# Performance work log

Hardware: AMD Instinct MI355X
Metric: run time of the kernel (lower is better)

## Reference

```python
import jax, jax.numpy as jnp
import numpy as np
import math

L, D, NH, DFF, RPE = 6, 256, 8, 1024, 512
HD = D // NH
B, NQ = 2, 300
FH, FW = 64, 64
N = FH * FW
STRIDE = 16
SCALE = 1.0 / math.sqrt(HD)


def _ln(x, w, b, eps=1e-5):
    m = jnp.mean(x, -1, keepdims=True)
    v = jnp.mean((x - m) ** 2, -1, keepdims=True)
    return (x - m) * jax.lax.rsqrt(v + eps) * w + b


def _mha_self(x, pos, in_w, in_b, out_w, out_b):
    # torch nn.MultiheadAttention with packed in_proj, q=k=x+pos, v=x
    qk = x + pos
    wq, wk, wv = jnp.split(in_w, 3, 0)
    bq, bk, bv = jnp.split(in_b, 3, 0)
    q = (qk @ wq.T + bq).reshape(B, NQ, NH, HD)
    k = (qk @ wk.T + bk).reshape(B, NQ, NH, HD)
    v = (x @ wv.T + bv).reshape(B, NQ, NH, HD)
    a = jax.nn.softmax(jnp.einsum('bqhd,bkhd->bhqk', q, k) * SCALE, -1)
    o = jnp.einsum('bhqk,bkhd->bqhd', a, v).reshape(B, NQ, D)
    return o @ out_w.T + out_b


def _cross(q_in, box, k_in, v_in, qw, qb, kw, kb, vw, vb, pw, pb,
           c1w1, c1b1, c1w2, c2w1, c2b1, c2w2):
    # box: [B,NQ,1,4] xyxy in absolute pixels; learned relative position bias
    pos_x = (jnp.arange(FW, dtype=jnp.float32) + 0.5) * STRIDE  # linspace(0.5,w-0.5,w)*stride
    pos_y = (jnp.arange(FH, dtype=jnp.float32) + 0.5) * STRIDE
    dx = box[..., 0::2] - pos_x[None, None, :, None]  # [B,NQ,FW,2]
    dy = box[..., 1::2] - pos_y[None, None, :, None]  # [B,NQ,FH,2]
    rpe_x = jax.nn.relu(dx @ c1w1.T + c1b1) @ c1w2.T  # [B,NQ,FW,NH]
    rpe_y = jax.nn.relu(dy @ c2w1.T + c2b1) @ c2w2.T  # [B,NQ,FH,NH]
    rpe = (rpe_y[:, :, :, None, :] + rpe_x[:, :, None, :, :]).reshape(B, NQ, N, NH)
    q = ((q_in @ qw.T + qb) * SCALE).reshape(B, NQ, NH, HD)
    k = (k_in @ kw.T + kb).reshape(B, N, NH, HD)
    v = (v_in @ vw.T + vb).reshape(B, N, NH, HD)
    attn = jnp.einsum('bqhd,bkhd->bhqk', q, k) + rpe.transpose(0, 3, 1, 2)
    a = jax.nn.softmax(attn, -1)
    o = jnp.einsum('bhqk,bkhd->bqhd', a, v).reshape(B, NQ, D)
    return o @ pw.T + pb


def _decoder(tgt, query_pos, reference_points, src, src_pos_embed,
             sa_in_w, sa_in_b, sa_out_w, sa_out_b, n1_w, n1_b,
             ca_q_w, ca_q_b, ca_k_w, ca_k_b, ca_v_w, ca_v_b, ca_proj_w, ca_proj_b,
             cpb1_w1, cpb1_b1, cpb1_w2, cpb2_w1, cpb2_b1, cpb2_w2,
             n2_w, n2_b, ffn_w1, ffn_b1, ffn_w2, ffn_b2, n3_w, n3_b):
    ref = reference_points[:, :, None]  # [B,NQ,1,4] cxcywh
    box = jnp.concatenate([ref[..., :2] - ref[..., 2:] * 0.5,
                           ref[..., :2] + ref[..., 2:] * 0.5], -1)
    kv = src + src_pos_embed
    out = tgt
    for i in range(L):  # post-norm decoder layers, dropout=0 (eval)
        t = _mha_self(out, query_pos, sa_in_w[i], sa_in_b[i], sa_out_w[i], sa_out_b[i])
        out = _ln(out + t, n1_w[i], n1_b[i])
        t = _cross(out + query_pos, box, kv, src,
                   ca_q_w[i], ca_q_b[i], ca_k_w[i], ca_k_b[i], ca_v_w[i], ca_v_b[i],
                   ca_proj_w[i], ca_proj_b[i], cpb1_w1[i], cpb1_b1[i], cpb1_w2[i],
                   cpb2_w1[i], cpb2_b1[i], cpb2_w2[i])
        out = _ln(out + t, n2_w[i], n2_b[i])
        t = jax.nn.relu(out @ ffn_w1[i].T + ffn_b1[i]) @ ffn_w2[i].T + ffn_b2[i]
        out = _ln(out + t, n3_w[i], n3_b[i])
    return out


def setup_inputs() -> dict:
    key = jax.random.key(0)
    ks = iter(jax.random.split(key, 64))
    def w(*shape, s=0.02):
        return jax.random.normal(next(ks), shape, jnp.float32) * s
    inp = {}
    inp['tgt'] = w(B, NQ, D, s=1.0)
    inp['query_pos'] = w(B, NQ, D, s=1.0)
    cxcy = jax.random.uniform(next(ks), (B, NQ, 2)) * (FW * STRIDE)
    wh = jax.random.uniform(next(ks), (B, NQ, 2)) * 256.0 + 16.0
    inp['reference_points'] = jnp.concatenate([cxcy, wh], -1)
    inp['src'] = w(B, N, D, s=1.0)
    inp['src_pos_embed'] = w(B, N, D, s=1.0)
    inp['src_spatial_shapes'] = jnp.array([[FH, FW]], jnp.int32)
    inp['sa_in_w'] = w(L, 3 * D, D); inp['sa_in_b'] = jnp.zeros((L, 3 * D))
    inp['sa_out_w'] = w(L, D, D); inp['sa_out_b'] = jnp.zeros((L, D))
    inp['n1_w'] = jnp.ones((L, D)); inp['n1_b'] = jnp.zeros((L, D))
    inp['ca_q_w'] = w(L, D, D); inp['ca_q_b'] = jnp.zeros((L, D))
    inp['ca_k_w'] = w(L, D, D); inp['ca_k_b'] = jnp.zeros((L, D))
    inp['ca_v_w'] = w(L, D, D); inp['ca_v_b'] = jnp.zeros((L, D))
    inp['ca_proj_w'] = w(L, D, D); inp['ca_proj_b'] = jnp.zeros((L, D))
    inp['cpb1_w1'] = w(L, RPE, 2, s=0.001); inp['cpb1_b1'] = jnp.zeros((L, RPE))
    inp['cpb1_w2'] = w(L, NH, RPE, s=0.001)
    inp['cpb2_w1'] = w(L, RPE, 2, s=0.001); inp['cpb2_b1'] = jnp.zeros((L, RPE))
    inp['cpb2_w2'] = w(L, NH, RPE, s=0.001)
    inp['n2_w'] = jnp.ones((L, D)); inp['n2_b'] = jnp.zeros((L, D))
    inp['ffn_w1'] = w(L, DFF, D); inp['ffn_b1'] = jnp.zeros((L, DFF))
    inp['ffn_w2'] = w(L, D, DFF); inp['ffn_b2'] = jnp.zeros((L, D))
    inp['n3_w'] = jnp.ones((L, D)); inp['n3_b'] = jnp.zeros((L, D))
    return inp


def reference(tgt, query_pos, reference_points, src, src_pos_embed, src_spatial_shapes,
              sa_in_w, sa_in_b, sa_out_w, sa_out_b, n1_w, n1_b,
              ca_q_w, ca_q_b, ca_k_w, ca_k_b, ca_v_w, ca_v_b, ca_proj_w, ca_proj_b,
              cpb1_w1, cpb1_b1, cpb1_w2, cpb2_w1, cpb2_b1, cpb2_w2,
              n2_w, n2_b, ffn_w1, ffn_b1, ffn_w2, ffn_b2, n3_w, n3_b):
    # src_spatial_shapes is static ([[FH, FW]]); dims closed over as constants.
    return _decoder(tgt, query_pos, reference_points, src, src_pos_embed,
                    sa_in_w, sa_in_b, sa_out_w, sa_out_b, n1_w, n1_b,
                    ca_q_w, ca_q_b, ca_k_w, ca_k_b, ca_v_w, ca_v_b, ca_proj_w, ca_proj_b,
                    cpb1_w1, cpb1_b1, cpb1_w2, cpb2_w1, cpb2_b1, cpb2_w2,
                    n2_w, n2_b, ffn_w1, ffn_b1, ffn_w2, ffn_b2, n3_w, n3_b)
```

## Files before the change

kernel.cpp:

```cpp
#include <hip/hip_runtime.h>
#include <math.h>

#define NQ   300
#define DMODEL 256
#define NHEAD 8
#define HDIM 32
#define BB   2
#define NKV  4096
#define RPEH 512
#define NLAYER 6
#define ATTN_SCALE 0.17677669529663687f

typedef short short8 __attribute__((ext_vector_type(8)));
typedef float f32x4 __attribute__((ext_vector_type(4)));
typedef unsigned short ushort_t;

__device__ __forceinline__ short f2bf(float f) {
    union { float fv; unsigned u; } v; v.fv = f;
    unsigned r = v.u + 0x7FFFu + ((v.u >> 16) & 1u);
    return (short)(r >> 16);
}
__device__ __forceinline__ float bf2f(ushort_t u) {
    union { unsigned u; float f; } v; v.u = ((unsigned)u) << 16;
    return v.f;
}
__device__ __forceinline__ short8 pack_bf8(float4 x, float4 y) {
    short8 v;
    v[0] = f2bf(x.x); v[1] = f2bf(x.y); v[2] = f2bf(x.z); v[3] = f2bf(x.w);
    v[4] = f2bf(y.x); v[5] = f2bf(y.y); v[6] = f2bf(y.z); v[7] = f2bf(y.w);
    return v;
}

__global__ __launch_bounds__(256) void prep_kernel(
    const float* __restrict__ src, const float* __restrict__ spe,
    const float* __restrict__ tgt, const float* __restrict__ qpos,
    const float* __restrict__ refp,
    ushort_t* __restrict__ kvb16, ushort_t* __restrict__ srcb16,
    float* __restrict__ outb, ushort_t* __restrict__ ob16,
    ushort_t* __restrict__ oq16,
    float* __restrict__ boxx, float* __restrict__ boxy)
{
    int i = blockIdx.x * 256 + threadIdx.x;
    if (i < BB * NKV * DMODEL) {
        float s = src[i];
        kvb16[i]  = (ushort_t)f2bf(s + spe[i]);
        srcb16[i] = (ushort_t)f2bf(s);
    }
    if (i < BB * NQ * DMODEL) {
        float tv = tgt[i];
        outb[i] = tv;
        ob16[i] = (ushort_t)f2bf(tv);
        oq16[i] = (ushort_t)f2bf(tv + qpos[i]);
    }
    if (i < BB * NQ) {
        float cx = refp[i * 4 + 0], cy = refp[i * 4 + 1];
        float w  = refp[i * 4 + 2], h  = refp[i * 4 + 3];
        boxx[i * 2 + 0] = cx - 0.5f * w;
        boxx[i * 2 + 1] = cx + 0.5f * w;
        boxy[i * 2 + 0] = cy - 0.5f * h;
        boxy[i * 2 + 1] = cy + 0.5f * h;
    }
}

__global__ __launch_bounds__(256) void wconv_kernel(
    const float* __restrict__ sain, const float* __restrict__ saout,
    const float* __restrict__ caq, const float* __restrict__ cak,
    const float* __restrict__ cav, const float* __restrict__ cap,
    const float* __restrict__ f1, const float* __restrict__ f2,
    ushort_t* __restrict__ dst)
{
    size_t i = ((size_t)blockIdx.x * 256 + threadIdx.x) * 8;
    if (i >= 6291456) return;
    const float* s; size_t off;
    if      (i < 1179648) { s = sain;  off = i; }
    else if (i < 1572864) { s = saout; off = i - 1179648; }
    else if (i < 1966080) { s = caq;   off = i - 1572864; }
    else if (i < 2359296) { s = cak;   off = i - 1966080; }
    else if (i < 2752512) { s = cav;   off = i - 2359296; }
    else if (i < 3145728) { s = cap;   off = i - 2752512; }
    else if (i < 4718592) { s = f1;    off = i - 3145728; }
    else                  { s = f2;    off = i - 4718592; }
    float4 x = *(const float4*)&s[off];
    float4 y = *(const float4*)&s[off + 4];
    *(short8*)&dst[i] = pack_bf8(x, y);
}

__global__ __launch_bounds__(256) void kv_mega(
    const ushort_t* __restrict__ kvb16, const ushort_t* __restrict__ srcb16,
    const ushort_t* __restrict__ Wk, const ushort_t* __restrict__ Wv,
    const float* __restrict__ kbias, const float* __restrict__ vbias,
    ushort_t* __restrict__ Kcb, ushort_t* __restrict__ Vcb)
{
    __shared__ short A_s[64][264];
    const int t = threadIdx.x;
    const int lane = t & 63, w = t >> 6;
    const int wr = w >> 1, wc = w & 1;
    const int l15 = lane & 15, lhi8 = (lane >> 4) * 8;
    const int n0 = blockIdx.x * 64;
    const int m0 = blockIdx.y * 64;
    const int sel = blockIdx.z;
    const ushort_t* A  = sel ? srcb16 : kvb16;
    const ushort_t* Wb = sel ? Wv : Wk;
    const float* bb    = sel ? vbias : kbias;
    ushort_t* Cb       = sel ? Vcb : Kcb;

    {
        int row = t >> 2, c0 = (t & 3) * 64;
        const ushort_t* ap = &A[(size_t)(m0 + row) * 256 + c0];
#pragma unroll
        for (int c8 = 0; c8 < 8; ++c8)
            *(short8*)&A_s[row][c0 + c8 * 8] = *(const short8*)(ap + c8 * 8);
    }
    __syncthreads();

    const int ar0 = wr * 32 + l15, ar1 = ar0 + 16;
    const int rowb = m0 + wr * 32 + (lane >> 4) * 4;
    const int colb = n0 + wc * 32 + l15;

    for (int l = 0; l < NLAYER; ++l) {
        const ushort_t* wp0 = &Wb[(size_t)l * 65536 + (size_t)(n0 + wc * 32 + l15) * 256 + lhi8];
        const ushort_t* wp1 = wp0 + 16 * 256;
        f32x4 acc[2][2];
#pragma unroll
        for (int i = 0; i < 2; ++i)
#pragma unroll
            for (int j = 0; j < 2; ++j)
#pragma unroll
                for (int r = 0; r < 4; ++r) acc[i][j][r] = 0.f;
#pragma unroll
        for (int k0 = 0; k0 < 256; k0 += 32) {
            short8 a0 = *(short8*)&A_s[ar0][k0 + lhi8];
            short8 a1 = *(short8*)&A_s[ar1][k0 + lhi8];
            short8 b0 = *(const short8*)(wp0 + k0);
            short8 b1 = *(const short8*)(wp1 + k0);
            acc[0][0] = __builtin_amdgcn_mfma_f32_16x16x32_bf16(a0, b0, acc[0][0], 0, 0, 0);
            acc[0][1] = __builtin_amdgcn_mfma_f32_16x16x32_bf16(a0, b1, acc[0][1], 0, 0, 0);
            acc[1][0] = __builtin_amdgcn_mfma_f32_16x16x32_bf16(a1, b0, acc[1][0], 0, 0, 0);
            acc[1][1] = __builtin_amdgcn_mfma_f32_16x16x32_bf16(a1, b1, acc[1][1], 0, 0, 0);
        }
        ushort_t* C = Cb + (size_t)l * (BB * NKV * DMODEL);
        const float* bl = bb + l * 256;
#pragma unroll
        for (int ni = 0; ni < 2; ++ni) {
            int col = colb + ni * 16;
            float bv = bl[col];
#pragma unroll
            for (int mi = 0; mi < 2; ++mi)
#pragma unroll
                for (int r = 0; r < 4; ++r) {
                    int row = rowb + mi * 16 + r;
                    C[(size_t)row * 256 + col] = (ushort_t)f2bf(acc[mi][ni][r] + bv);
                }
        }
    }
}

template<int OUT_BF16, int RELU>
__global__ __launch_bounds__(256) void gemm_direct(
    const ushort_t* __restrict__ A1, const ushort_t* __restrict__ A2, int plimit,
    int lda, const ushort_t* __restrict__ W, const float* __restrict__ bias,
    void* __restrict__ Cv, int ldc, int M, int K, float scale, int slimit)
{
    const int t = threadIdx.x;
    const int lane = t & 63, w = t >> 6;
    const int wr = w >> 1, wc = w & 1;
    const int l15 = lane & 15, lhi8 = (lane >> 4) * 8;
    const int m0 = blockIdx.y * 64, n0 = blockIdx.x * 64;
    const ushort_t* A = (n0 < plimit) ? A1 : A2;

    int r0 = m0 + wr * 32 + l15;      if (r0 > M - 1) r0 = M - 1;
    int r1 = m0 + wr * 32 + 16 + l15; if (r1 > M - 1) r1 = M - 1;
    const ushort_t* ap0 = &A[(size_t)r0 * lda + lhi8];
    const ushort_t* ap1 = &A[(size_t)r1 * lda + lhi8];
    const ushort_t* wp0 = &W[(size_t)(n0 + wc * 32 + l15) * K + lhi8];
    const ushort_t* wp1 = wp0 + (size_t)16 * K;

    f32x4 acc[2][2];
#pragma unroll
    for (int i = 0; i < 2; ++i)
#pragma unroll
        for (int j = 0; j < 2; ++j)
#pragma unroll
            for (int r = 0; r < 4; ++r) acc[i][j][r] = 0.f;

    for (int k0 = 0; k0 < K; k0 += 32) {
        short8 a0 = *(const short8*)(ap0 + k0);
        short8 a1 = *(const short8*)(ap1 + k0);
        short8 b0 = *(const short8*)(wp0 + k0);
        short8 b1 = *(const short8*)(wp1 + k0);
        acc[0][0] = __builtin_amdgcn_mfma_f32_16x16x32_bf16(a0, b0, acc[0][0], 0, 0, 0);
        acc[0][1] = __builtin_amdgcn_mfma_f32_16x16x32_bf16(a0, b1, acc[0][1], 0, 0, 0);
        acc[1][0] = __builtin_amdgcn_mfma_f32_16x16x32_bf16(a1, b0, acc[1][0], 0, 0, 0);
        acc[1][1] = __builtin_amdgcn_mfma_f32_16x16x32_bf16(a1, b1, acc[1][1], 0, 0, 0);
    }

    const int rowb = m0 + wr * 32 + (lane >> 4) * 4;
    const int colb = n0 + wc * 32 + l15;
#pragma unroll
    for (int ni = 0; ni < 2; ++ni) {
        int col = colb + ni * 16;
        float bv = bias[col];
#pragma unroll
        for (int mi = 0; mi < 2; ++mi)
#pragma unroll
            for (int r = 0; r < 4; ++r) {
                int row = rowb + mi * 16 + r;
                if (row < M) {
                    float v = acc[mi][ni][r] + bv;
                    if (col < slimit) v *= scale;
                    if (RELU) v = fmaxf(v, 0.f);
                    if (OUT_BF16)
                        ((ushort_t*)Cv)[(size_t)row * ldc + col] = (ushort_t)f2bf(v);
                    else
                        ((float*)Cv)[(size_t)row * ldc + col] = v;
                }
            }
    }
}

__global__ __launch_bounds__(256) void ln_residual(
    float* __restrict__ out, const float* __restrict__ tt,
    const float* __restrict__ qpos,
    const float* __restrict__ w, const float* __restrict__ b,
    ushort_t* __restrict__ ob16, ushort_t* __restrict__ oq16, int rows)
{
    const int wid = threadIdx.x >> 6, lane = threadIdx.x & 63;
    const int row = blockIdx.x * 4 + wid;
    if (row >= rows) return;
    const float* orow = out + row * DMODEL;
    const float* trow = tt + row * DMODEL;
    float x[4];
#pragma unroll
    for (int i = 0; i < 4; ++i) x[i] = orow[lane + 64 * i] + trow[lane + 64 * i];
    float s = x[0] + x[1] + x[2] + x[3];
#pragma unroll
    for (int mask = 1; mask < 64; mask <<= 1) s += __shfl_xor(s, mask);
    float mean = s * (1.f / 256.f);
    float vs = 0.f;
#pragma unroll
    for (int i = 0; i < 4; ++i) { float d = x[i] - mean; vs += d * d; }
#pragma unroll
    for (int mask = 1; mask < 64; mask <<= 1) vs += __shfl_xor(vs, mask);
    float r = rsqrtf(vs * (1.f / 256.f) + 1e-5f);
    float* orw = out + row * DMODEL;
#pragma unroll
    for (int i = 0; i < 4; ++i) {
        int c = lane + 64 * i;
        float val = (x[i] - mean) * r * w[c] + b[c];
        orw[c] = val;
        ob16[row * DMODEL + c] = (ushort_t)f2bf(val);
        oq16[row * DMODEL + c] = (ushort_t)f2bf(val + qpos[row * DMODEL + c]);
    }
}

__global__ __launch_bounds__(256) void rpe_all(
    const float* __restrict__ boxx, const float* __restrict__ boxy,
    const float* __restrict__ cpb1_w1, const float* __restrict__ cpb1_b1,
    const float* __restrict__ cpb1_w2,
    const float* __restrict__ cpb2_w1, const float* __restrict__ cpb2_b1,
    const float* __restrict__ cpb2_w2,
    float* __restrict__ rx6, float* __restrict__ ry6)
{
    __shared__ float wb_s[RPEH][4];
    __shared__ float w2_s[RPEH][8];

    const int axis = blockIdx.y;
    const int l = blockIdx.z;
    const float* __restrict__ w1 = (axis ? cpb2_w1 : cpb1_w1) + (size_t)l * 1024;
    const float* __restrict__ b1 = (axis ? cpb2_b1 : cpb1_b1) + (size_t)l * 512;
    const float* __restrict__ w2 = (axis ? cpb2_w2 : cpb1_w2) + (size_t)l * 4096;
    const float* __restrict__ bx = axis ? boxy : boxx;
    const int t = threadIdx.x;

    for (int j = t; j < RPEH; j += 256) {
        wb_s[j][0] = w1[2 * j];
        wb_s[j][1] = w1[2 * j + 1];
        wb_s[j][2] = b1[j];
        wb_s[j][3] = 0.f;
#pragma unroll
        for (int h = 0; h < 8; ++h) w2_s[j][h] = w2[h * RPEH + j];
    }
    __syncthreads();

    const int row = blockIdx.x * 256 + t;
    const int i  = row & 63;
    const int bq = row >> 6;
    const float pos = (i + 0.5f) * 16.0f;
    const float d0 = bx[bq * 2 + 0] - pos;
    const float d1 = bx[bq * 2 + 1] - pos;

    float acc[8];
#pragma unroll
    for (int h = 0; h < 8; ++h) acc[h] = 0.f;

#pragma unroll 4
    for (int j = 0; j < RPEH; ++j) {
        float4 wb = *(const float4*)&wb_s[j][0];
        float hv = fmaxf(fmaf(d0, wb.x, fmaf(d1, wb.y, wb.z)), 0.f);
        float4 a = *(const float4*)&w2_s[j][0];
        float4 c = *(const float4*)&w2_s[j][4];
        acc[0] = fmaf(hv, a.x, acc[0]);
        acc[1] = fmaf(hv, a.y, acc[1]);
        acc[2] = fmaf(hv, a.z, acc[2]);
        acc[3] = fmaf(hv, a.w, acc[3]);
        acc[4] = fmaf(hv, c.x, acc[4]);
        acc[5] = fmaf(hv, c.y, acc[5]);
        acc[6] = fmaf(hv, c.z, acc[6]);
        acc[7] = fmaf(hv, c.w, acc[7]);
    }

    const int b = bq / NQ, q = bq % NQ;
    float* __restrict__ dst = (axis ? ry6 : rx6) + (size_t)l * 307200;
#pragma unroll
    for (int h = 0; h < 8; ++h)
        dst[((size_t)(b * NHEAD + h) * NQ + q) * 64 + i] = acc[h];
}

template<int HAS_RPE>
__global__ __launch_bounds__(256) void attn_mfma(
    const ushort_t* __restrict__ Q, int ldq,
    const ushort_t* __restrict__ K, int ldk,
    const ushort_t* __restrict__ V, int ldv,
    int nkeys, int kps,
    const float* __restrict__ RX, const float* __restrict__ RY,
    ushort_t* __restrict__ po, float* __restrict__ pm, float* __restrict__ pl,
    int nsplit)
{
    __shared__ short Q_s[64][40];
    __shared__ short K_s[64][40];
    __shared__ short V_s[32][72];
    __shared__ short P_s[4][16][72];

    const int t = threadIdx.x;
    const int lane = t & 63, w = t >> 6;
    const int l15 = lane & 15, lhi8 = (lane >> 4) * 8, lhi4 = (lane >> 4) * 4;
    const int bh = blockIdx.y, b = bh >> 3, h = bh & 7;
    const int q0 = blockIdx.x * 64;
    const int sp = blockIdx.z;

    {
        int q = t >> 2, kc = (t & 3) * 8;
        int qi = q0 + q;
        short8 qv = {0,0,0,0,0,0,0,0};
        if (qi < NQ) qv = *(const short8*)&Q[((size_t)(b * NQ + qi)) * ldq + h * HDIM + kc];
        *(short8*)&Q_s[q][kc] = qv;
    }

    float rxv[4][4];
    const float* ryp[4];
    if (HAS_RPE) {
#pragma unroll
        for (int r = 0; r < 4; ++r) {
            int qi = q0 + w * 16 + lhi4 + r;
            int qc = qi < NQ ? qi : NQ - 1;
            const float* rxp = &RX[((size_t)bh * NQ + qc) * 64];
            ryp[r] = &RY[((size_t)bh * NQ + qc) * 64];
#pragma unroll
            for (int nf = 0; nf < 4; ++nf) rxv[r][nf] = rxp[nf * 16 + l15];
        }
    }

    float m_r[4], l_r[4];
    f32x4 oacc[2];
#pragma unroll
    for (int r = 0; r < 4; ++r) { m_r[r] = -1e30f; l_r[r] = 0.f; }
#pragma unroll
    for (int ni = 0; ni < 2; ++ni)
#pragma unroll
        for (int r = 0; r < 4; ++r) oacc[ni][r] = 0.f;

    const int nt = kps >> 6;
    for (int kt = 0; kt < nt; ++kt) {
        const int key0 = sp * kps + (kt << 6);
        __syncthreads();
        {
            int key = t >> 2, kc = (t & 3) * 8;
            int rk = key0 + key;
            int rkc = rk < nkeys ? rk : nkeys - 1;
            short8 kvv = *(const short8*)&K[((size_t)(b * nkeys + rkc)) * ldk + h * HDIM + kc];
            *(short8*)&K_s[key][kc] = kvv;
            short8 vvv = *(const short8*)&V[((size_t)(b * nkeys + rkc)) * ldv + h * HDIM + kc];
#pragma unroll
            for (int j = 0; j < 8; ++j) V_s[kc + j][key] = vvv[j];
        }
        __syncthreads();

        short8 aq = *(short8*)&Q_s[w * 16 + l15][lhi8];
        f32x4 sacc[4];
#pragma unroll
        for (int nf = 0; nf < 4; ++nf) {
#pragma unroll
            for (int r = 0; r < 4; ++r) sacc[nf][r] = 0.f;
            short8 kb = *(short8*)&K_s[nf * 16 + l15][lhi8];
            sacc[nf] = __builtin_amdgcn_mfma_f32_16x16x32_bf16(aq, kb, sacc[nf], 0, 0, 0);
        }

        const int ktg = key0 >> 6;
        const bool kv0 = key0 +      l15 < nkeys;
        const bool kv1 = key0 + 16 + l15 < nkeys;
        const bool kv2 = key0 + 32 + l15 < nkeys;
        const bool kv3 = key0 + 48 + l15 < nkeys;
        float c_r[4];
#pragma unroll
        for (int r = 0; r < 4; ++r) {
            float ryv = HAS_RPE ? ryp[r][ktg] : 0.f;
            float sv0 = sacc[0][r] + ryv, sv1 = sacc[1][r] + ryv;
            float sv2 = sacc[2][r] + ryv, sv3 = sacc[3][r] + ryv;
            if (HAS_RPE) {
                sv0 += rxv[r][0]; sv1 += rxv[r][1];
                sv2 += rxv[r][2]; sv3 += rxv[r][3];
            }
            sv0 = kv0 ? sv0 : -1e30f;
            sv1 = kv1 ? sv1 : -1e30f;
            sv2 = kv2 ? sv2 : -1e30f;
            sv3 = kv3 ? sv3 : -1e30f;
            float tmax = fmaxf(fmaxf(sv0, sv1), fmaxf(sv2, sv3));
#pragma unroll
            for (int mask = 1; mask < 16; mask <<= 1)
                tmax = fmaxf(tmax, __shfl_xor(tmax, mask));
            float mn = fmaxf(m_r[r], tmax);
            float cc = __expf(m_r[r] - mn);
            m_r[r] = mn; c_r[r] = cc;
            float p0 = __expf(sv0 - mn), p1 = __expf(sv1 - mn);
            float p2 = __expf(sv2 - mn), p3 = __expf(sv3 - mn);
            float ps = p0 + p1 + p2 + p3;
#pragma unroll
            for (int mask = 1; mask < 16; mask <<= 1) ps += __shfl_xor(ps, mask);
            l_r[r] = l_r[r] * cc + ps;
            P_s[w][lhi4 + r][     l15] = f2bf(p0);
            P_s[w][lhi4 + r][16 + l15] = f2bf(p1);
            P_s[w][lhi4 + r][32 + l15] = f2bf(p2);
            P_s[w][lhi4 + r][48 + l15] = f2bf(p3);
        }
#pragma unroll
        for (int ni = 0; ni < 2; ++ni)
#pragma unroll
            for (int r = 0; r < 4; ++r) oacc[ni][r] *= c_r[r];

        short8 pa0 = *(short8*)&P_s[w][l15][lhi8];
        short8 pa1 = *(short8*)&P_s[w][l15][32 + lhi8];
#pragma unroll
        for (int ni = 0; ni < 2; ++ni) {
            short8 vb0 = *(short8*)&V_s[ni * 16 + l15][lhi8];
            short8 vb1 = *(short8*)&V_s[ni * 16 + l15][32 + lhi8];
            oacc[ni] = __builtin_amdgcn_mfma_f32_16x16x32_bf16(pa0, vb0, oacc[ni], 0, 0, 0);
            oacc[ni] = __builtin_amdgcn_mfma_f32_16x16x32_bf16(pa1, vb1, oacc[ni], 0, 0, 0);
        }
    }

#pragma unroll
    for (int r = 0; r < 4; ++r) {
        int qi = q0 + w * 16 + lhi4 + r;
        if (qi < NQ) {
            size_t base = ((size_t)(bh * nsplit + sp) * NQ + qi);
            if (l15 == 0) { pm[base] = m_r[r]; pl[base] = l_r[r]; }
            po[base * 32 + l15] = (ushort_t)f2bf(oacc[0][r]);
            po[base * 32 + 16 + l15] = (ushort_t)f2bf(oacc[1][r]);
        }
    }
}

__global__ __launch_bounds__(256) void combine_gemm(
    const ushort_t* __restrict__ po, const float* __restrict__ pm,
    const float* __restrict__ pl, int nsplit,
    const ushort_t* __restrict__ W, const float* __restrict__ bias,
    float* __restrict__ C, int M)
{
    __shared__ short A_s2[64][264];
    const int t = threadIdx.x;
    const int m0 = blockIdx.y * 64, n0 = blockIdx.x * 64;

    {
        int rloc = t >> 2;
        int row = m0 + rloc;
        int dc = (t & 3) * 64;
        if (row < M) {
            int b = row / NQ, q = row % NQ;
#pragma unroll
            for (int hh = 0; hh < 2; ++hh) {
                int h = (dc >> 5) + hh;
                int bh = b * NHEAD + h;
                float Mx = -1e30f;
                for (int s = 0; s < nsplit; ++s)
                    Mx = fmaxf(Mx, pm[(size_t)(bh * nsplit + s) * NQ + q]);
                float L = 0.f;
                float acc[32];
#pragma unroll
                for (int d = 0; d < 32; ++d) acc[d] = 0.f;
                for (int s = 0; s < nsplit; ++s) {
                    size_t base = (size_t)(bh * nsplit + s) * NQ + q;
                    float wgt = __expf(pm[base] - Mx);
                    L += pl[base] * wgt;
                    const ushort_t* pp = &po[base * 32];
#pragma unroll
                    for (int d = 0; d < 32; ++d) acc[d] += bf2f(pp[d]) * wgt;
                }
                float inv = 1.f / L;
#pragma unroll
                for (int d = 0; d < 32; ++d)
                    A_s2[rloc][dc + hh * 32 + d] = f2bf(acc[d] * inv);
            }
        } else {
#pragma unroll
            for (int d = 0; d < 64; ++d) A_s2[rloc][dc + d] = 0;
        }
    }
    __syncthreads();

    const int lane = t & 63, w = t >> 6;
    const int wr = w >> 1, wc = w & 1;
    const int l15 = lane & 15, lhi8 = (lane >> 4) * 8;
    const ushort_t* wp0 = &W[(size_t)(n0 + wc * 32 + l15) * 256 + lhi8];
    const ushort_t* wp1 = wp0 + 16 * 256;
    f32x4 acc[2][2];
#pragma unroll
    for (int i = 0; i < 2; ++i)
#pragma unroll
        for (int j = 0; j < 2; ++j)
#pragma unroll
            for (int r = 0; r < 4; ++r) acc[i][j][r] = 0.f;

#pragma unroll
    for (int k0 = 0; k0 < 256; k0 += 32) {
        short8 a0 = *(short8*)&A_s2[wr * 32 + l15][k0 + lhi8];
        short8 a1 = *(short8*)&A_s2[wr * 32 + 16 + l15][k0 + lhi8];
        short8 b0 = *(const short8*)(wp0 + k0);
        short8 b1 = *(const short8*)(wp1 + k0);
        acc[0][0] = __builtin_amdgcn_mfma_f32_16x16x32_bf16(a0, b0, acc[0][0], 0, 0, 0);
        acc[0][1] = __builtin_amdgcn_mfma_f32_16x16x32_bf16(a0, b1, acc[0][1], 0, 0, 0);
        acc[1][0] = __builtin_amdgcn_mfma_f32_16x16x32_bf16(a1, b0, acc[1][0], 0, 0, 0);
        acc[1][1] = __builtin_amdgcn_mfma_f32_16x16x32_bf16(a1, b1, acc[1][1], 0, 0, 0);
    }

    const int rowb = m0 + wr * 32 + (lane >> 4) * 4;
    const int colb = n0 + wc * 32 + l15;
#pragma unroll
    for (int ni = 0; ni < 2; ++ni) {
        int col = colb + ni * 16;
        float bv = bias[col];
#pragma unroll
        for (int mi = 0; mi < 2; ++mi)
#pragma unroll
            for (int r = 0; r < 4; ++r) {
                int row = rowb + mi * 16 + r;
                if (row < M)
                    C[(size_t)row * 256 + col] = acc[mi][ni][r] + bv;
            }
    }
}

extern "C" void kernel_launch(void* const* d_in, const int* in_sizes, int n_in,
                              void* d_out, int out_size, void* d_ws, size_t ws_size,
                              hipStream_t stream)
{
    const float* tgt   = (const float*)d_in[0];
    const float* qpos  = (const float*)d_in[1];
    const float* refp  = (const float*)d_in[2];
    const float* src   = (const float*)d_in[3];
    const float* spe   = (const float*)d_in[4];
    const float* sa_in_w  = (const float*)d_in[6];
    const float* sa_in_b  = (const float*)d_in[7];
    const float* sa_out_w = (const float*)d_in[8];
    const float* sa_out_b = (const float*)d_in[9];
    const float* n1_w  = (const float*)d_in[10];
    const float* n1_b  = (const float*)d_in[11];
    const float* ca_q_w = (const float*)d_in[12];
    const float* ca_q_b = (const float*)d_in[13];
    const float* ca_k_w = (const float*)d_in[14];
    const float* ca_k_b = (const float*)d_in[15];
    const float* ca_v_w = (const float*)d_in[16];
    const float* ca_v_b = (const float*)d_in[17];
    const float* ca_p_w = (const float*)d_in[18];
    const float* ca_p_b = (const float*)d_in[19];
    const float* cpb1_w1 = (const float*)d_in[20];
    const float* cpb1_b1 = (const float*)d_in[21];
    const float* cpb1_w2 = (const float*)d_in[22];
    const float* cpb2_w1 = (const float*)d_in[23];
    const float* cpb2_b1 = (const float*)d_in[24];
    const float* cpb2_w2 = (const float*)d_in[25];
    const float* n2_w = (const float*)d_in[26];
    const float* n2_b = (const float*)d_in[27];
    const float* ffn_w1 = (const float*)d_in[28];
    const float* ffn_b1 = (const float*)d_in[29];
    const float* ffn_w2 = (const float*)d_in[30];
    const float* ffn_b2 = (const float*)d_in[31];
    const float* n3_w = (const float*)d_in[32];
    const float* n3_b = (const float*)d_in[33];

    float* ws  = (float*)d_ws;
    float* outb = ws;
    float* tb   = outb + 153600;
    float* rx6  = tb + 153600;
    float* ry6  = rx6 + 1843200;
    float* boxx = ry6 + 1843200;
    float* boxy = boxx + 1200;
    float* pm   = boxy + 1200;
    float* pl   = pm + 38400;
    ushort_t* u = (ushort_t*)(pl + 38400);
    ushort_t* qkvb   = u;
    ushort_t* qcb    = qkvb + 460800;
    ushort_t* ob16   = qcb + 153600;
    ushort_t* oq16   = ob16 + 153600;
    ushort_t* hbb    = oq16 + 153600;
    ushort_t* poh    = hbb + 614400;
    ushort_t* kvb16  = poh + 1228800;
    ushort_t* srcb16 = kvb16 + 2097152;
    ushort_t* Kcb    = srcb16 + 2097152;
    ushort_t* Vcb    = Kcb + 12582912;
    ushort_t* Wseg   = Vcb + 12582912;
    ushort_t* Wsain  = Wseg;
    ushort_t* Wsaout = Wsain + 1179648;
    ushort_t* Wcaq   = Wsaout + 393216;
    ushort_t* Wcak   = Wcaq + 393216;
    ushort_t* Wcav   = Wcak + 393216;
    ushort_t* Wcap   = Wcav + 393216;
    ushort_t* Wff1   = Wcap + 393216;
    ushort_t* Wff2   = Wff1 + 1572864;

    const int M = BB * NQ;

    prep_kernel<<<8192, 256, 0, stream>>>(src, spe, tgt, qpos, refp,
        kvb16, srcb16, outb, ob16, oq16, boxx, boxy);
    wconv_kernel<<<3072, 256, 0, stream>>>(sa_in_w, sa_out_w, ca_q_w, ca_k_w,
        ca_v_w, ca_p_w, ffn_w1, ffn_w2, Wseg);
    rpe_all<<<dim3(150, 2, 6), 256, 0, stream>>>(boxx, boxy,
        cpb1_w1, cpb1_b1, cpb1_w2, cpb2_w1, cpb2_b1, cpb2_w2, rx6, ry6);
    kv_mega<<<dim3(4, 128, 2), 256, 0, stream>>>(kvb16, srcb16, Wcak, Wcav,
        ca_k_b, ca_v_b, Kcb, Vcb);

    for (int l = 0; l < NLAYER; ++l) {
        gemm_direct<1,0><<<dim3(12, 10), 256, 0, stream>>>(
            oq16, ob16, 512, 256, Wsain + (size_t)l * 196608, sa_in_b + (size_t)l * 768,
            qkvb, 768, M, 256, ATTN_SCALE, 256);
        attn_mfma<0><<<dim3(5, 16, 5), 256, 0, stream>>>(
            qkvb, 768, qkvb + 256, 768, qkvb + 512, 768,
            NQ, 64, nullptr, nullptr, poh, pm, pl, 5);
        combine_gemm<<<dim3(4, 10), 256, 0, stream>>>(
            poh, pm, pl, 5, Wsaout + (size_t)l * 65536, sa_out_b + l * 256, tb, M);
        ln_residual<<<150, 256, 0, stream>>>(outb, tb, qpos,
            n1_w + l * 256, n1_b + l * 256, ob16, oq16, M);

        gemm_direct<1,0><<<dim3(4, 10), 256, 0, stream>>>(
            oq16, oq16, 256, 256, Wcaq + (size_t)l * 65536, ca_q_b + l * 256,
            qcb, 256, M, 256, ATTN_SCALE, 256);
        attn_mfma<1><<<dim3(5, 16, 8), 256, 0, stream>>>(
            qcb, 256, Kcb + (size_t)l * 2097152, 256, Vcb + (size_t)l * 2097152, 256,
            NKV, 512, rx6 + (size_t)l * 307200, ry6 + (size_t)l * 307200,
            poh, pm, pl, 8);
        combine_gemm<<<dim3(4, 10), 256, 0, stream>>>(
            poh, pm, pl, 8, Wcap + (size_t)l * 65536, ca_p_b + l * 256, tb, M);
        ln_residual<<<150, 256, 0, stream>>>(outb, tb, qpos,
            n2_w + l * 256, n2_b + l * 256, ob16, oq16, M);

        gemm_direct<1,1><<<dim3(16, 10), 256, 0, stream>>>(
            ob16, ob16, 1024, 256, Wff1 + (size_t)l * 262144, ffn_b1 + l * 1024,
            hbb, 1024, M, 256, 1.f, 0);
        gemm_direct<0,0><<<dim3(4, 10), 256, 0, stream>>>(
            hbb, hbb, 256, 1024, Wff2 + (size_t)l * 262144, ffn_b2 + l * 256,
            tb, 256, M, 1024, 1.f, 0);
        ln_residual<<<150, 256, 0, stream>>>(outb, tb, qpos,
            n3_w + l * 256, n3_b + l * 256, ob16, oq16, M);
    }

    hipMemcpyAsync(d_out, outb, (size_t)M * DMODEL * sizeof(float),
                   hipMemcpyDeviceToDevice, stream);
}
```

Baseline: 866.4 us.

## Fuse output projections with residual LayerNorm and restructure RPE MLP evaluation

The attention output projections and the second FFN GEMM now each compute a full 64x256 row tile per block and apply residual add plus LayerNorm in the same kernel. This removes the separate ln_residual launches and the round trip of the intermediate tensor through global memory, 18 launches in total. In exchange the grid shrinks from 40 blocks to 10 for these GEMMs, so far fewer compute units are used. The RPE kernel now has each thread evaluate 8 consecutive positions by stepping the pre-activation linearly, which cuts the first-layer math and enables vectorised stores, but launches far fewer blocks.

```diff
diff --git a/kernel.cpp b/kernel.cpp
--- a/kernel.cpp
+++ b/kernel.cpp
@@ -218,41 +218,6 @@
     }
 }
 
-__global__ __launch_bounds__(256) void ln_residual(
-    float* __restrict__ out, const float* __restrict__ tt,
-    const float* __restrict__ qpos,
-    const float* __restrict__ w, const float* __restrict__ b,
-    ushort_t* __restrict__ ob16, ushort_t* __restrict__ oq16, int rows)
-{
-    const int wid = threadIdx.x >> 6, lane = threadIdx.x & 63;
-    const int row = blockIdx.x * 4 + wid;
-    if (row >= rows) return;
-    const float* orow = out + row * DMODEL;
-    const float* trow = tt + row * DMODEL;
-    float x[4];
-#pragma unroll
-    for (int i = 0; i < 4; ++i) x[i] = orow[lane + 64 * i] + trow[lane + 64 * i];
-    float s = x[0] + x[1] + x[2] + x[3];
-#pragma unroll
-    for (int mask = 1; mask < 64; mask <<= 1) s += __shfl_xor(s, mask);
-    float mean = s * (1.f / 256.f);
-    float vs = 0.f;
-#pragma unroll
-    for (int i = 0; i < 4; ++i) { float d = x[i] - mean; vs += d * d; }
-#pragma unroll
-    for (int mask = 1; mask < 64; mask <<= 1) vs += __shfl_xor(vs, mask);
-    float r = rsqrtf(vs * (1.f / 256.f) + 1e-5f);
-    float* orw = out + row * DMODEL;
-#pragma unroll
-    for (int i = 0; i < 4; ++i) {
-        int c = lane + 64 * i;
-        float val = (x[i] - mean) * r * w[c] + b[c];
-        orw[c] = val;
-        ob16[row * DMODEL + c] = (ushort_t)f2bf(val);
-        oq16[row * DMODEL + c] = (ushort_t)f2bf(val + qpos[row * DMODEL + c]);
-    }
-}
-
 __global__ __launch_bounds__(256) void rpe_all(
     const float* __restrict__ boxx, const float* __restrict__ boxy,
     const float* __restrict__ cpb1_w1, const float* __restrict__ cpb1_b1,
@@ -282,38 +247,53 @@
     }
     __syncthreads();
 
-    const int row = blockIdx.x * 256 + t;
-    const int i  = row & 63;
-    const int bq = row >> 6;
-    const float pos = (i + 0.5f) * 16.0f;
-    const float d0 = bx[bq * 2 + 0] - pos;
-    const float d1 = bx[bq * 2 + 1] - pos;
-
-    float acc[8];
-#pragma unroll
-    for (int h = 0; h < 8; ++h) acc[h] = 0.f;
-
-#pragma unroll 4
+    const int bq = blockIdx.x * 32 + (t >> 3);
+    const int i0 = (t & 7) * 8;
+    const bool valid = bq < BB * NQ;
+    const int bqc = valid ? bq : BB * NQ - 1;
+    const float pos0 = (i0 + 0.5f) * 16.0f;
+    const float d0 = bx[bqc * 2 + 0] - pos0;
+    const float d1 = bx[bqc * 2 + 1] - pos0;
+
+    float acc[8][8];
+#pragma unroll
+    for (int e = 0; e < 8; ++e)
+#pragma unroll
+        for (int h = 0; h < 8; ++h) acc[e][h] = 0.f;
+
+#pragma unroll 2
     for (int j = 0; j < RPEH; ++j) {
         float4 wb = *(const float4*)&wb_s[j][0];
-        float hv = fmaxf(fmaf(d0, wb.x, fmaf(d1, wb.y, wb.z)), 0.f);
-        float4 a = *(const float4*)&w2_s[j][0];
-        float4 c = *(const float4*)&w2_s[j][4];
-        acc[0] = fmaf(hv, a.x, acc[0]);
-        acc[1] = fmaf(hv, a.y, acc[1]);
-        acc[2] = fmaf(hv, a.z, acc[2]);
-        acc[3] = fmaf(hv, a.w, acc[3]);
-        acc[4] = fmaf(hv, c.x, acc[4]);
-        acc[5] = fmaf(hv, c.y, acc[5]);
-        acc[6] = fmaf(hv, c.z, acc[6]);
-        acc[7] = fmaf(hv, c.w, acc[7]);
-    }
-
-    const int b = bq / NQ, q = bq % NQ;
-    float* __restrict__ dst = (axis ? ry6 : rx6) + (size_t)l * 307200;
-#pragma unroll
-    for (int h = 0; h < 8; ++h)
-        dst[((size_t)(b * NHEAD + h) * NQ + q) * 64 + i] = acc[h];
+        float a = fmaf(d0, wb.x, fmaf(d1, wb.y, wb.z));
+        float s = 16.0f * (wb.x + wb.y);
+        float4 w2a = *(const float4*)&w2_s[j][0];
+        float4 w2b = *(const float4*)&w2_s[j][4];
+        float tv = a;
+#pragma unroll
+        for (int e = 0; e < 8; ++e) {
+            float hv = fmaxf(tv, 0.f);
+            acc[e][0] = fmaf(hv, w2a.x, acc[e][0]);
+            acc[e][1] = fmaf(hv, w2a.y, acc[e][1]);
+            acc[e][2] = fmaf(hv, w2a.z, acc[e][2]);
+            acc[e][3] = fmaf(hv, w2a.w, acc[e][3]);
+            acc[e][4] = fmaf(hv, w2b.x, acc[e][4]);
+            acc[e][5] = fmaf(hv, w2b.y, acc[e][5]);
+            acc[e][6] = fmaf(hv, w2b.z, acc[e][6]);
+            acc[e][7] = fmaf(hv, w2b.w, acc[e][7]);
+            tv -= s;
+        }
+    }
+
+    if (valid) {
+        const int b = bq / NQ, q = bq % NQ;
+        float* __restrict__ dst = (axis ? ry6 : rx6) + (size_t)l * 307200;
+#pragma unroll
+        for (int h = 0; h < 8; ++h) {
+            float* p = &dst[((size_t)(b * NHEAD + h) * NQ + q) * 64 + i0];
+            *(float4*)p       = make_float4(acc[0][h], acc[1][h], acc[2][h], acc[3][h]);
+            *(float4*)(p + 4) = make_float4(acc[4][h], acc[5][h], acc[6][h], acc[7][h]);
+        }
+    }
 }
 
 template<int HAS_RPE>
@@ -460,15 +440,18 @@
     }
 }
 
-__global__ __launch_bounds__(256) void combine_gemm(
+__global__ __launch_bounds__(256) void combine_gemm_ln(
     const ushort_t* __restrict__ po, const float* __restrict__ pm,
     const float* __restrict__ pl, int nsplit,
     const ushort_t* __restrict__ W, const float* __restrict__ bias,
-    float* __restrict__ C, int M)
+    float* __restrict__ outb, const float* __restrict__ qpos,
+    const float* __restrict__ lnw, const float* __restrict__ lnb,
+    ushort_t* __restrict__ ob16, ushort_t* __restrict__ oq16, int M)
 {
     __shared__ short A_s2[64][264];
+    __shared__ float C_s[64][260];
     const int t = threadIdx.x;
-    const int m0 = blockIdx.y * 64, n0 = blockIdx.x * 64;
+    const int m0 = blockIdx.x * 64;
 
     {
         int rloc = t >> 2;
@@ -484,21 +467,21 @@
                 for (int s = 0; s < nsplit; ++s)
                     Mx = fmaxf(Mx, pm[(size_t)(bh * nsplit + s) * NQ + q]);
                 float L = 0.f;
-                float acc[32];
-#pragma unroll
-                for (int d = 0; d < 32; ++d) acc[d] = 0.f;
+                float acc1[32];
+#pragma unroll
+                for (int d = 0; d < 32; ++d) acc1[d] = 0.f;
                 for (int s = 0; s < nsplit; ++s) {
                     size_t base = (size_t)(bh * nsplit + s) * NQ + q;
                     float wgt = __expf(pm[base] - Mx);
                     L += pl[base] * wgt;
                     const ushort_t* pp = &po[base * 32];
 #pragma unroll
-                    for (int d = 0; d < 32; ++d) acc[d] += bf2f(pp[d]) * wgt;
+                    for (int d = 0; d < 32; ++d) acc1[d] += bf2f(pp[d]) * wgt;
                 }
                 float inv = 1.f / L;
 #pragma unroll
                 for (int d = 0; d < 32; ++d)
-                    A_s2[rloc][dc + hh * 32 + d] = f2bf(acc[d] * inv);
+                    A_s2[rloc][dc + hh * 32 + d] = f2bf(acc1[d] * inv);
             }
         } else {
 #pragma unroll
@@ -510,42 +493,162 @@
     const int lane = t & 63, w = t >> 6;
     const int wr = w >> 1, wc = w & 1;
     const int l15 = lane & 15, lhi8 = (lane >> 4) * 8;
-    const ushort_t* wp0 = &W[(size_t)(n0 + wc * 32 + l15) * 256 + lhi8];
-    const ushort_t* wp1 = wp0 + 16 * 256;
-    f32x4 acc[2][2];
-#pragma unroll
-    for (int i = 0; i < 2; ++i)
-#pragma unroll
-        for (int j = 0; j < 2; ++j)
-#pragma unroll
-            for (int r = 0; r < 4; ++r) acc[i][j][r] = 0.f;
-
+    f32x4 acc[4][2][2];
+#pragma unroll
+    for (int a = 0; a < 4; ++a)
+#pragma unroll
+        for (int i = 0; i < 2; ++i)
+#pragma unroll
+            for (int j = 0; j < 2; ++j)
+#pragma unroll
+                for (int r = 0; r < 4; ++r) acc[a][i][j][r] = 0.f;
+
+    const int ar0 = wr * 32 + l15, ar1 = ar0 + 16;
 #pragma unroll
     for (int k0 = 0; k0 < 256; k0 += 32) {
-        short8 a0 = *(short8*)&A_s2[wr * 32 + l15][k0 + lhi8];
-        short8 a1 = *(short8*)&A_s2[wr * 32 + 16 + l15][k0 + lhi8];
-        short8 b0 = *(const short8*)(wp0 + k0);
-        short8 b1 = *(const short8*)(wp1 + k0);
-        acc[0][0] = __builtin_amdgcn_mfma_f32_16x16x32_bf16(a0, b0, acc[0][0], 0, 0, 0);
-        acc[0][1] = __builtin_amdgcn_mfma_f32_16x16x32_bf16(a0, b1, acc[0][1], 0, 0, 0);
-        acc[1][0] = __builtin_amdgcn_mfma_f32_16x16x32_bf16(a1, b0, acc[1][0], 0, 0, 0);
-        acc[1][1] = __builtin_amdgcn_mfma_f32_16x16x32_bf16(a1, b1, acc[1][1], 0, 0, 0);
-    }
-
-    const int rowb = m0 + wr * 32 + (lane >> 4) * 4;
-    const int colb = n0 + wc * 32 + l15;
-#pragma unroll
-    for (int ni = 0; ni < 2; ++ni) {
-        int col = colb + ni * 16;
-        float bv = bias[col];
-#pragma unroll
-        for (int mi = 0; mi < 2; ++mi)
-#pragma unroll
-            for (int r = 0; r < 4; ++r) {
-                int row = rowb + mi * 16 + r;
-                if (row < M)
-                    C[(size_t)row * 256 + col] = acc[mi][ni][r] + bv;
-            }
+        short8 a0 = *(short8*)&A_s2[ar0][k0 + lhi8];
+        short8 a1 = *(short8*)&A_s2[ar1][k0 + lhi8];
+#pragma unroll
+        for (int n0i = 0; n0i < 4; ++n0i) {
+            const ushort_t* wp0 = &W[(size_t)(n0i * 64 + wc * 32 + l15) * 256 + k0 + lhi8];
+            short8 b0 = *(const short8*)wp0;
+            short8 b1 = *(const short8*)(wp0 + 16 * 256);
+            acc[n0i][0][0] = __builtin_amdgcn_mfma_f32_16x16x32_bf16(a0, b0, acc[n0i][0][0], 0, 0, 0);
+            acc[n0i][0][1] = __builtin_amdgcn_mfma_f32_16x16x32_bf16(a0, b1, acc[n0i][0][1], 0, 0, 0);
+            acc[n0i][1][0] = __builtin_amdgcn_mfma_f32_16x16x32_bf16(a1, b0, acc[n0i][1][0], 0, 0, 0);
+            acc[n0i][1][1] = __builtin_amdgcn_mfma_f32_16x16x32_bf16(a1, b1, acc[n0i][1][1], 0, 0, 0);
+        }
+    }
+    const int rowl = wr * 32 + (lane >> 4) * 4;
+#pragma unroll
+    for (int n0i = 0; n0i < 4; ++n0i)
+#pragma unroll
+        for (int ni = 0; ni < 2; ++ni) {
+            int col = n0i * 64 + wc * 32 + ni * 16 + l15;
+            float bv = bias[col];
+#pragma unroll
+            for (int mi = 0; mi < 2; ++mi)
+#pragma unroll
+                for (int r = 0; r < 4; ++r)
+                    C_s[rowl + mi * 16 + r][col] = acc[n0i][mi][ni][r] + bv;
+        }
+    __syncthreads();
+
+    const int wid = t >> 6, lv = t & 63;
+    for (int k = 0; k < 16; ++k) {
+        int rloc = wid * 16 + k;
+        int row = m0 + rloc;
+        if (row >= M) break;
+        float x[4];
+#pragma unroll
+        for (int i = 0; i < 4; ++i)
+            x[i] = outb[row * DMODEL + lv + 64 * i] + C_s[rloc][lv + 64 * i];
+        float s = x[0] + x[1] + x[2] + x[3];
+#pragma unroll
+        for (int mask = 1; mask < 64; mask <<= 1) s += __shfl_xor(s, mask);
+        float mean = s * (1.f / 256.f);
+        float vs = 0.f;
+#pragma unroll
+        for (int i = 0; i < 4; ++i) { float d = x[i] - mean; vs += d * d; }
+#pragma unroll
+        for (int mask = 1; mask < 64; mask <<= 1) vs += __shfl_xor(vs, mask);
+        float rv = rsqrtf(vs * (1.f / 256.f) + 1e-5f);
+#pragma unroll
+        for (int i = 0; i < 4; ++i) {
+            int c = lv + 64 * i;
+            float val = (x[i] - mean) * rv * lnw[c] + lnb[c];
+            outb[row * DMODEL + c] = val;
+            ob16[row * DMODEL + c] = (ushort_t)f2bf(val);
+            oq16[row * DMODEL + c] = (ushort_t)f2bf(val + qpos[row * DMODEL + c]);
+        }
+    }
+}
+
+__global__ __launch_bounds__(256) void ffn2_ln(
+    const ushort_t* __restrict__ A, const ushort_t* __restrict__ W,
+    const float* __restrict__ bias,
+    float* __restrict__ outb, const float* __restrict__ qpos,
+    const float* __restrict__ lnw, const float* __restrict__ lnb,
+    ushort_t* __restrict__ ob16, ushort_t* __restrict__ oq16, int M)
+{
+    __shared__ float C_s[64][260];
+    const int t = threadIdx.x;
+    const int m0 = blockIdx.x * 64;
+    const int lane = t & 63, w = t >> 6;
+    const int wr = w >> 1, wc = w & 1;
+    const int l15 = lane & 15, lhi8 = (lane >> 4) * 8;
+
+    int r0 = m0 + wr * 32 + l15;      if (r0 > M - 1) r0 = M - 1;
+    int r1 = m0 + wr * 32 + 16 + l15; if (r1 > M - 1) r1 = M - 1;
+    const ushort_t* ap0 = &A[(size_t)r0 * 1024 + lhi8];
+    const ushort_t* ap1 = &A[(size_t)r1 * 1024 + lhi8];
+
+    f32x4 acc[4][2][2];
+#pragma unroll
+    for (int a = 0; a < 4; ++a)
+#pragma unroll
+        for (int i = 0; i < 2; ++i)
+#pragma unroll
+            for (int j = 0; j < 2; ++j)
+#pragma unroll
+                for (int r = 0; r < 4; ++r) acc[a][i][j][r] = 0.f;
+
+    for (int k0 = 0; k0 < 1024; k0 += 32) {
+        short8 a0 = *(const short8*)(ap0 + k0);
+        short8 a1 = *(const short8*)(ap1 + k0);
+#pragma unroll
+        for (int n0i = 0; n0i < 4; ++n0i) {
+            const ushort_t* wp0 = &W[(size_t)(n0i * 64 + wc * 32 + l15) * 1024 + k0 + lhi8];
+            short8 b0 = *(const short8*)wp0;
+            short8 b1 = *(const short8*)(wp0 + 16 * 1024);
+            acc[n0i][0][0] = __builtin_amdgcn_mfma_f32_16x16x32_bf16(a0, b0, acc[n0i][0][0], 0, 0, 0);
+            acc[n0i][0][1] = __builtin_amdgcn_mfma_f32_16x16x32_bf16(a0, b1, acc[n0i][0][1], 0, 0, 0);
+            acc[n0i][1][0] = __builtin_amdgcn_mfma_f32_16x16x32_bf16(a1, b0, acc[n0i][1][0], 0, 0, 0);
+            acc[n0i][1][1] = __builtin_amdgcn_mfma_f32_16x16x32_bf16(a1, b1, acc[n0i][1][1], 0, 0, 0);
+        }
+    }
+    const int rowl = wr * 32 + (lane >> 4) * 4;
+#pragma unroll
+    for (int n0i = 0; n0i < 4; ++n0i)
+#pragma unroll
+        for (int ni = 0; ni < 2; ++ni) {
+            int col = n0i * 64 + wc * 32 + ni * 16 + l15;
+            float bv = bias[col];
+#pragma unroll
+            for (int mi = 0; mi < 2; ++mi)
+#pragma unroll
+                for (int r = 0; r < 4; ++r)
+                    C_s[rowl + mi * 16 + r][col] = acc[n0i][mi][ni][r] + bv;
+        }
+    __syncthreads();
+
+    const int wid = t >> 6, lv = t & 63;
+    for (int k = 0; k < 16; ++k) {
+        int rloc = wid * 16 + k;
+        int row = m0 + rloc;
+        if (row >= M) break;
+        float x[4];
+#pragma unroll
+        for (int i = 0; i < 4; ++i)
+            x[i] = outb[row * DMODEL + lv + 64 * i] + C_s[rloc][lv + 64 * i];
+        float s = x[0] + x[1] + x[2] + x[3];
+#pragma unroll
+        for (int mask = 1; mask < 64; mask <<= 1) s += __shfl_xor(s, mask);
+        float mean = s * (1.f / 256.f);
+        float vs = 0.f;
+#pragma unroll
+        for (int i = 0; i < 4; ++i) { float d = x[i] - mean; vs += d * d; }
+#pragma unroll
+        for (int mask = 1; mask < 64; mask <<= 1) vs += __shfl_xor(vs, mask);
+        float rv = rsqrtf(vs * (1.f / 256.f) + 1e-5f);
+#pragma unroll
+        for (int i = 0; i < 4; ++i) {
+            int c = lv + 64 * i;
+            float val = (x[i] - mean) * rv * lnw[c] + lnb[c];
+            outb[row * DMODEL + c] = val;
+            ob16[row * DMODEL + c] = (ushort_t)f2bf(val);
+            oq16[row * DMODEL + c] = (ushort_t)f2bf(val + qpos[row * DMODEL + c]);
+        }
     }
 }
 
@@ -623,7 +726,7 @@
         kvb16, srcb16, outb, ob16, oq16, boxx, boxy);
     wconv_kernel<<<3072, 256, 0, stream>>>(sa_in_w, sa_out_w, ca_q_w, ca_k_w,
         ca_v_w, ca_p_w, ffn_w1, ffn_w2, Wseg);
-    rpe_all<<<dim3(150, 2, 6), 256, 0, stream>>>(boxx, boxy,
+    rpe_all<<<dim3(19, 2, 6), 256, 0, stream>>>(boxx, boxy,
         cpb1_w1, cpb1_b1, cpb1_w2, cpb2_w1, cpb2_b1, cpb2_w2, rx6, ry6);
     kv_mega<<<dim3(4, 128, 2), 256, 0, stream>>>(kvb16, srcb16, Wcak, Wcav,
         ca_k_b, ca_v_b, Kcb, Vcb);
@@ -635,10 +738,9 @@
         attn_mfma<0><<<dim3(5, 16, 5), 256, 0, stream>>>(
             qkvb, 768, qkvb + 256, 768, qkvb + 512, 768,
             NQ, 64, nullptr, nullptr, poh, pm, pl, 5);
-        combine_gemm<<<dim3(4, 10), 256, 0, stream>>>(
-            poh, pm, pl, 5, Wsaout + (size_t)l * 65536, sa_out_b + l * 256, tb, M);
-        ln_residual<<<150, 256, 0, stream>>>(outb, tb, qpos,
-            n1_w + l * 256, n1_b + l * 256, ob16, oq16, M);
+        combine_gemm_ln<<<10, 256, 0, stream>>>(
+            poh, pm, pl, 5, Wsaout + (size_t)l * 65536, sa_out_b + l * 256,
+            outb, qpos, n1_w + l * 256, n1_b + l * 256, ob16, oq16, M);
 
         gemm_direct<1,0><<<dim3(4, 10), 256, 0, stream>>>(
             oq16, oq16, 256, 256, Wcaq + (size_t)l * 65536, ca_q_b + l * 256,
@@ -647,19 +749,16 @@
             qcb, 256, Kcb + (size_t)l * 2097152, 256, Vcb + (size_t)l * 2097152, 256,
             NKV, 512, rx6 + (size_t)l * 307200, ry6 + (size_t)l * 307200,
             poh, pm, pl, 8);
-        combine_gemm<<<dim3(4, 10), 256, 0, stream>>>(
-            poh, pm, pl, 8, Wcap + (size_t)l * 65536, ca_p_b + l * 256, tb, M);
-        ln_residual<<<150, 256, 0, stream>>>(outb, tb, qpos,
-            n2_w + l * 256, n2_b + l * 256, ob16, oq16, M);
+        combine_gemm_ln<<<10, 256, 0, stream>>>(
+            poh, pm, pl, 8, Wcap + (size_t)l * 65536, ca_p_b + l * 256,
+            outb, qpos, n2_w + l * 256, n2_b + l * 256, ob16, oq16, M);
 
         gemm_direct<1,1><<<dim3(16, 10), 256, 0, stream>>>(
             ob16, ob16, 1024, 256, Wff1 + (size_t)l * 262144, ffn_b1 + l * 1024,
             hbb, 1024, M, 256, 1.f, 0);
-        gemm_direct<0,0><<<dim3(4, 10), 256, 0, stream>>>(
-            hbb, hbb, 256, 1024, Wff2 + (size_t)l * 262144, ffn_b2 + l * 256,
-            tb, 256, M, 1024, 1.f, 0);
-        ln_residual<<<150, 256, 0, stream>>>(outb, tb, qpos,
-            n3_w + l * 256, n3_b + l * 256, ob16, oq16, M);
+        ffn2_ln<<<10, 256, 0, stream>>>(
+            hbb, Wff2 + (size_t)l * 262144, ffn_b2 + l * 256,
+            outb, qpos, n3_w + l * 256, n3_b + l * 256, ob16, oq16, M);
     }
 
     hipMemcpyAsync(d_out, outb, (size_t)M * DMODEL * sizeof(float),
```

Result: slower. 1.227 ms (+41.6%).

## Compute RPE MLP second layer with bf16 MFMA, one block per query

Applied to the files above, without the earlier changes.

Rewrites the relative-position-bias MLP kernel so each block handles one (batch, query) row with its 64 positions. The first layer is folded algebraically per query (w·box + b minus pos·sum(w)), and the 512-wide hidden-to-heads projection runs on 16x16x32 bf16 MFMA instead of scalar FMAs, with the 8 heads padded to 16. This cuts the scalar FMA work of a kernel that handles 6 layers x 2 axes up front, at the cost of bf16 rounding of the hidden activations and weights, wasted MFMA columns, and four times as many blocks, each restaging the weights. An accumulator in the combine kernel is also renamed.

```diff
diff --git a/kernel.cpp b/kernel.cpp
--- a/kernel.cpp
+++ b/kernel.cpp
@@ -261,9 +261,10 @@
     const float* __restrict__ cpb2_w2,
     float* __restrict__ rx6, float* __restrict__ ry6)
 {
-    __shared__ float wb_s[RPEH][4];
-    __shared__ float w2_s[RPEH][8];
-
+    __shared__ __align__(16) float2 as2_s[RPEH];
+    __shared__ short w2b_s[8][520];
+
+    const int bq = blockIdx.x;
     const int axis = blockIdx.y;
     const int l = blockIdx.z;
     const float* __restrict__ w1 = (axis ? cpb2_w1 : cpb1_w1) + (size_t)l * 1024;
@@ -272,48 +273,59 @@
     const float* __restrict__ bx = axis ? boxy : boxx;
     const int t = threadIdx.x;
 
+    const float x0 = bx[bq * 2 + 0], x1 = bx[bq * 2 + 1];
+
     for (int j = t; j < RPEH; j += 256) {
-        wb_s[j][0] = w1[2 * j];
-        wb_s[j][1] = w1[2 * j + 1];
-        wb_s[j][2] = b1[j];
-        wb_s[j][3] = 0.f;
-#pragma unroll
-        for (int h = 0; h < 8; ++h) w2_s[j][h] = w2[h * RPEH + j];
+        float2 wp = *(const float2*)&w1[2 * j];
+        as2_s[j] = make_float2(fmaf(wp.x, x0, fmaf(wp.y, x1, b1[j])),
+                               wp.x + wp.y);
+    }
+    {
+        int h = t >> 5, j16 = (t & 31) * 16;
+        const float* wp = &w2[h * RPEH + j16];
+        float4 a = *(const float4*)wp;
+        float4 b = *(const float4*)(wp + 4);
+        float4 c = *(const float4*)(wp + 8);
+        float4 d = *(const float4*)(wp + 12);
+        *(short8*)&w2b_s[h][j16]     = pack_bf8(a, b);
+        *(short8*)&w2b_s[h][j16 + 8] = pack_bf8(c, d);
     }
     __syncthreads();
 
-    const int row = blockIdx.x * 256 + t;
-    const int i  = row & 63;
-    const int bq = row >> 6;
-    const float pos = (i + 0.5f) * 16.0f;
-    const float d0 = bx[bq * 2 + 0] - pos;
-    const float d1 = bx[bq * 2 + 1] - pos;
-
-    float acc[8];
-#pragma unroll
-    for (int h = 0; h < 8; ++h) acc[h] = 0.f;
+    const int lane = t & 63, w = t >> 6;
+    const int l15 = lane & 15, lhi8 = (lane >> 4) * 8, lhi4 = (lane >> 4) * 4;
+    const float pos_i = ((w * 16 + l15) + 0.5f) * 16.0f;
+
+    f32x4 acc;
+#pragma unroll
+    for (int r = 0; r < 4; ++r) acc[r] = 0.f;
 
 #pragma unroll 4
-    for (int j = 0; j < RPEH; ++j) {
-        float4 wb = *(const float4*)&wb_s[j][0];
-        float hv = fmaxf(fmaf(d0, wb.x, fmaf(d1, wb.y, wb.z)), 0.f);
-        float4 a = *(const float4*)&w2_s[j][0];
-        float4 c = *(const float4*)&w2_s[j][4];
-        acc[0] = fmaf(hv, a.x, acc[0]);
-        acc[1] = fmaf(hv, a.y, acc[1]);
-        acc[2] = fmaf(hv, a.z, acc[2]);
-        acc[3] = fmaf(hv, a.w, acc[3]);
-        acc[4] = fmaf(hv, c.x, acc[4]);
-        acc[5] = fmaf(hv, c.y, acc[5]);
-        acc[6] = fmaf(hv, c.z, acc[6]);
-        acc[7] = fmaf(hv, c.w, acc[7]);
-    }
-
-    const int b = bq / NQ, q = bq % NQ;
-    float* __restrict__ dst = (axis ? ry6 : rx6) + (size_t)l * 307200;
-#pragma unroll
-    for (int h = 0; h < 8; ++h)
-        dst[((size_t)(b * NHEAD + h) * NQ + q) * 64 + i] = acc[h];
+    for (int k0 = 0; k0 < RPEH; k0 += 32) {
+        const int j0 = k0 + lhi8;
+        const float4* ap = (const float4*)&as2_s[j0];
+        float4 p0 = ap[0], p1 = ap[1], p2 = ap[2], p3 = ap[3];
+        short8 ha;
+        ha[0] = f2bf(fmaxf(fmaf(-pos_i, p0.y, p0.x), 0.f));
+        ha[1] = f2bf(fmaxf(fmaf(-pos_i, p0.w, p0.z), 0.f));
+        ha[2] = f2bf(fmaxf(fmaf(-pos_i, p1.y, p1.x), 0.f));
+        ha[3] = f2bf(fmaxf(fmaf(-pos_i, p1.w, p1.z), 0.f));
+        ha[4] = f2bf(fmaxf(fmaf(-pos_i, p2.y, p2.x), 0.f));
+        ha[5] = f2bf(fmaxf(fmaf(-pos_i, p2.w, p2.z), 0.f));
+        ha[6] = f2bf(fmaxf(fmaf(-pos_i, p3.y, p3.x), 0.f));
+        ha[7] = f2bf(fmaxf(fmaf(-pos_i, p3.w, p3.z), 0.f));
+        short8 wb;
+        if (l15 < 8) wb = *(short8*)&w2b_s[l15][j0];
+        else { short8 z = {0,0,0,0,0,0,0,0}; wb = z; }
+        acc = __builtin_amdgcn_mfma_f32_16x16x32_bf16(ha, wb, acc, 0, 0, 0);
+    }
+
+    if (l15 < 8) {
+        const int b = bq / NQ, q = bq % NQ;
+        float* __restrict__ dst = (axis ? ry6 : rx6) + (size_t)l * 307200;
+        float* p = &dst[((size_t)(b * NHEAD + l15) * NQ + q) * 64 + w * 16 + lhi4];
+        *(float4*)p = *(float4*)&acc;
+    }
 }
 
 template<int HAS_RPE>
@@ -484,21 +496,21 @@
                 for (int s = 0; s < nsplit; ++s)
                     Mx = fmaxf(Mx, pm[(size_t)(bh * nsplit + s) * NQ + q]);
                 float L = 0.f;
-                float acc[32];
-#pragma unroll
-                for (int d = 0; d < 32; ++d) acc[d] = 0.f;
+                float acc1[32];
+#pragma unroll
+                for (int d = 0; d < 32; ++d) acc1[d] = 0.f;
                 for (int s = 0; s < nsplit; ++s) {
                     size_t base = (size_t)(bh * nsplit + s) * NQ + q;
                     float wgt = __expf(pm[base] - Mx);
                     L += pl[base] * wgt;
                     const ushort_t* pp = &po[base * 32];
 #pragma unroll
-                    for (int d = 0; d < 32; ++d) acc[d] += bf2f(pp[d]) * wgt;
+                    for (int d = 0; d < 32; ++d) acc1[d] += bf2f(pp[d]) * wgt;
                 }
                 float inv = 1.f / L;
 #pragma unroll
                 for (int d = 0; d < 32; ++d)
-                    A_s2[rloc][dc + hh * 32 + d] = f2bf(acc[d] * inv);
+                    A_s2[rloc][dc + hh * 32 + d] = f2bf(acc1[d] * inv);
             }
         } else {
 #pragma unroll
@@ -623,7 +635,7 @@
         kvb16, srcb16, outb, ob16, oq16, boxx, boxy);
     wconv_kernel<<<3072, 256, 0, stream>>>(sa_in_w, sa_out_w, ca_q_w, ca_k_w,
         ca_v_w, ca_p_w, ffn_w1, ffn_w2, Wseg);
-    rpe_all<<<dim3(150, 2, 6), 256, 0, stream>>>(boxx, boxy,
+    rpe_all<<<dim3(600, 2, 6), 256, 0, stream>>>(boxx, boxy,
         cpb1_w1, cpb1_b1, cpb1_w2, cpb2_w1, cpb2_b1, cpb2_w2, rx6, ry6);
     kv_mega<<<dim3(4, 128, 2), 256, 0, stream>>>(kvb16, srcb16, Wcak, Wcav,
         ca_k_b, ca_v_b, Kcb, Vcb);
```

After: 782.7 us. 9.7% less time.
